# Kernel optimization log

Hardware: AMD Instinct MI355X
Metric: run time of the kernel (lower is better)

The kernel has to match this reference:

```python
import jax, jax.numpy as jnp
import numpy as np

EPS = 1e-5  # BatchNorm1d default eps


def setup_inputs() -> dict:
    key = jax.random.key(0)
    k1, k2 = jax.random.split(key)
    b, d, h, w = 32, 256, 32, 128
    x = jax.random.normal(k1, (b, d, h, w), dtype=jnp.float32)
    # mask=True means padded/masked position (excluded from stats, left untouched)
    mask = jax.random.randint(k2, (b, 1, h, w), 0, 2).astype(bool)
    gamma = jnp.ones((d,), dtype=jnp.float32)
    beta = jnp.zeros((d,), dtype=jnp.float32)
    return {"x": x, "mask": mask, "gamma": gamma, "beta": beta}


def reference(x, mask, gamma, beta):
    # x: [b, d, h, w], mask: [b, 1, h, w] (True = masked)
    not_mask = ~mask[:, 0]                      # [b, h, w]
    wgt = not_mask.astype(x.dtype)              # [b, h, w]
    count = jnp.maximum(wgt.sum(), jnp.asarray(1.0, x.dtype))
    xt = jnp.transpose(x, (0, 2, 3, 1))         # [b, h, w, d]
    wm = wgt[..., None]                         # [b, h, w, 1]
    # masked per-channel batch statistics (biased variance, as BN training mode)
    mean = (xt * wm).sum(axis=(0, 1, 2)) / count                  # [d]
    var = (wm * (xt - mean) ** 2).sum(axis=(0, 1, 2)) / count     # [d]
    normed = (xt - mean) * jax.lax.rsqrt(var + EPS) * gamma + beta
    out = jnp.where(not_mask[..., None], normed, xt)              # scatter-back
    return jnp.transpose(out, (0, 3, 1, 2))     # [b, d, h, w]
```

## Files before the change

kernel.cpp:

```cpp
#include <hip/hip_runtime.h>

#define BB 32
#define DD 256
#define HW 4096
#define DHW (DD * HW)
#define TOTAL (BB * DHW)
#define NSLICE (BB * DD)
#define EPS 1e-5f

typedef float floatx4 __attribute__((ext_vector_type(4)));


__global__ void __launch_bounds__(256)
stats_kernel(const float* __restrict__ x, const int* __restrict__ mask,
             float* __restrict__ ws) {
    const int slice = blockIdx.x;
    const int b = slice >> 8;
    const int d = slice & 255;
    const float4* xs = reinterpret_cast<const float4*>(
        x + (size_t)b * DHW + (size_t)d * HW);
    const int4* ms = reinterpret_cast<const int4*>(mask + b * HW);
    const int tid = threadIdx.x;

    float sum = 0.f, sq = 0.f, cnt = 0.f;
#pragma unroll
    for (int j = 0; j < 4; ++j) {
        const int v = j * 256 + tid;
        float4 xv = xs[v];
        int4 mv = ms[v];
        if (!mv.x) { sum += xv.x; sq += xv.x * xv.x; cnt += 1.f; }
        if (!mv.y) { sum += xv.y; sq += xv.y * xv.y; cnt += 1.f; }
        if (!mv.z) { sum += xv.z; sq += xv.z * xv.z; cnt += 1.f; }
        if (!mv.w) { sum += xv.w; sq += xv.w * xv.w; cnt += 1.f; }
    }

#pragma unroll
    for (int off = 32; off > 0; off >>= 1) {
        sum += __shfl_down(sum, off);
        sq  += __shfl_down(sq, off);
        cnt += __shfl_down(cnt, off);
    }

    __shared__ float ssum[4], ssq[4], scnt[4];
    const int wave = tid >> 6, lane = tid & 63;
    if (lane == 0) { ssum[wave] = sum; ssq[wave] = sq; scnt[wave] = cnt; }
    __syncthreads();
    if (tid == 0) {
        float ts = 0.f, tq = 0.f, tc = 0.f;
#pragma unroll
        for (int i = 0; i < 4; ++i) { ts += ssum[i]; tq += ssq[i]; tc += scnt[i]; }
        ws[slice] = ts;
        ws[NSLICE + slice] = tq;
        if (d == 0) ws[2 * NSLICE + b] = tc;
    }
}

__global__ void __launch_bounds__(256)
apply_kernel(const float* __restrict__ x, const int* __restrict__ mask,
             const float* __restrict__ ws, const float* __restrict__ gamma,
             const float* __restrict__ beta, float* __restrict__ out) {
    __shared__ float s_scale[DD], s_bias[DD];
    const int tid = threadIdx.x;

    float cnt = 0.f;
#pragma unroll
    for (int b = 0; b < BB; ++b) cnt += ws[2 * NSLICE + b];
    cnt = fmaxf(cnt, 1.0f);
    float sum = 0.f, sq = 0.f;
#pragma unroll
    for (int b = 0; b < BB; ++b) {
        sum += ws[b * DD + tid];
        sq  += ws[NSLICE + b * DD + tid];
    }
    const float mean = sum / cnt;
    const float var = fmaxf(sq / cnt - mean * mean, 0.0f);
    const float sc = rsqrtf(var + EPS) * gamma[tid];
    s_scale[tid] = sc;
    s_bias[tid] = beta[tid] - mean * sc;
    __syncthreads();

    const int nvec = TOTAL / 4;
    const int stride = gridDim.x * blockDim.x;
    floatx4* __restrict__ ov = reinterpret_cast<floatx4*>(out);
    for (int v = blockIdx.x * blockDim.x + tid; v < nvec; v += stride) {
        const int e = v << 2;
        const int b = e >> 20;
        const int rem = e & (DHW - 1);
        const int d = rem >> 12;
        const int pos = rem & 4095;
        float4 xv = reinterpret_cast<const float4*>(x)[v];
        int4 mv = reinterpret_cast<const int4*>(mask)[(b * HW + pos) >> 2];
        const float s = s_scale[d], bi = s_bias[d];
        floatx4 o;
        o.x = mv.x ? xv.x : xv.x * s + bi;
        o.y = mv.y ? xv.y : xv.y * s + bi;
        o.z = mv.z ? xv.z : xv.z * s + bi;
        o.w = mv.w ? xv.w : xv.w * s + bi;
        __builtin_nontemporal_store(o, &ov[v]);
    }
}

extern "C" void kernel_launch(void* const* d_in, const int* in_sizes, int n_in,
                              void* d_out, int out_size, void* d_ws, size_t ws_size,
                              hipStream_t stream) {
    const float* x     = (const float*)d_in[0];
    const int*   mask  = (const int*)d_in[1];
    const float* gamma = (const float*)d_in[2];
    const float* beta  = (const float*)d_in[3];
    float* out = (float*)d_out;
    float* ws  = (float*)d_ws;

    stats_kernel<<<NSLICE, 256, 0, stream>>>(x, mask, ws);
    apply_kernel<<<2048, 256, 0, stream>>>(x, mask, ws, gamma, beta, out);
}
```

Before: 70.00 us.

## Fuse stats and apply into one per-channel kernel with block-level reduction

Replaces the two-kernel stats/apply pipeline with a single kernel where each 1024-thread block owns one channel. The block reduces masked sum, sum of squares and count across all batches, computes scale and bias, then re-reads the same channel data to write the normalized output. This removes the workspace round-trip and the second launch, and aims to serve the second read of x from cache instead of HBM. In exchange, the grid is only 256 large blocks with one block per channel, which limits occupancy and latency hiding, and any benefit from the re-read depends on the cache holding the data.

New measurement: 64.93 us (median of 2 runs). 7.2% less time.

```diff
diff --git a/kernel.cpp b/kernel.cpp
--- a/kernel.cpp
+++ b/kernel.cpp
@@ -4,99 +4,74 @@
 #define DD 256
 #define HW 4096
 #define DHW (DD * HW)
-#define TOTAL (BB * DHW)
-#define NSLICE (BB * DD)
 #define EPS 1e-5f
 
 typedef float floatx4 __attribute__((ext_vector_type(4)));
 
+__global__ void __launch_bounds__(1024)
+channel_kernel(const float* __restrict__ x, const int* __restrict__ mask,
+               const float* __restrict__ gamma, const float* __restrict__ beta,
+               float* __restrict__ out) {
+    const int d = blockIdx.x;
+    const int tid = threadIdx.x;
+    const int wave = tid >> 6, lane = tid & 63;
 
-__global__ void __launch_bounds__(256)
-stats_kernel(const float* __restrict__ x, const int* __restrict__ mask,
-             float* __restrict__ ws) {
-    const int slice = blockIdx.x;
-    const int b = slice >> 8;
-    const int d = slice & 255;
-    const float4* xs = reinterpret_cast<const float4*>(
-        x + (size_t)b * DHW + (size_t)d * HW);
-    const int4* ms = reinterpret_cast<const int4*>(mask + b * HW);
-    const int tid = threadIdx.x;
+    const float4* __restrict__ xv4 = reinterpret_cast<const float4*>(x);
+    const int4*   __restrict__ mv4 = reinterpret_cast<const int4*>(mask);
+    const int xbase = d * 1024 + tid;
 
     float sum = 0.f, sq = 0.f, cnt = 0.f;
-#pragma unroll
-    for (int j = 0; j < 4; ++j) {
-        const int v = j * 256 + tid;
-        float4 xv = xs[v];
-        int4 mv = ms[v];
+#pragma unroll 8
+    for (int b = 0; b < BB; ++b) {
+        float4 xv = xv4[b * (DHW / 4) + xbase];
+        int4  mv = mv4[b * 1024 + tid];
         if (!mv.x) { sum += xv.x; sq += xv.x * xv.x; cnt += 1.f; }
         if (!mv.y) { sum += xv.y; sq += xv.y * xv.y; cnt += 1.f; }
         if (!mv.z) { sum += xv.z; sq += xv.z * xv.z; cnt += 1.f; }
         if (!mv.w) { sum += xv.w; sq += xv.w * xv.w; cnt += 1.f; }
     }
 
+    __shared__ float rsum[16], rsq[16], rcnt[16];
+    __shared__ float s_scale, s_bias;
 #pragma unroll
     for (int off = 32; off > 0; off >>= 1) {
         sum += __shfl_down(sum, off);
         sq  += __shfl_down(sq, off);
         cnt += __shfl_down(cnt, off);
     }
+    if (lane == 0) { rsum[wave] = sum; rsq[wave] = sq; rcnt[wave] = cnt; }
+    __syncthreads();
+    if (tid < 16) {
+        float ts = rsum[tid], tq = rsq[tid], tc = rcnt[tid];
+#pragma unroll
+        for (int off = 8; off > 0; off >>= 1) {
+            ts += __shfl_down(ts, off, 16);
+            tq += __shfl_down(tq, off, 16);
+            tc += __shfl_down(tc, off, 16);
+        }
+        if (tid == 0) {
+            tc = fmaxf(tc, 1.0f);
+            const float mean = ts / tc;
+            const float var = fmaxf(tq / tc - mean * mean, 0.0f);
+            const float sc = rsqrtf(var + EPS) * gamma[d];
+            s_scale = sc;
+            s_bias = beta[d] - mean * sc;
+        }
+    }
+    __syncthreads();
+    const float sc = s_scale, bi = s_bias;
 
-    __shared__ float ssum[4], ssq[4], scnt[4];
-    const int wave = tid >> 6, lane = tid & 63;
-    if (lane == 0) { ssum[wave] = sum; ssq[wave] = sq; scnt[wave] = cnt; }
-    __syncthreads();
-    if (tid == 0) {
-        float ts = 0.f, tq = 0.f, tc = 0.f;
-#pragma unroll
-        for (int i = 0; i < 4; ++i) { ts += ssum[i]; tq += ssq[i]; tc += scnt[i]; }
-        ws[slice] = ts;
-        ws[NSLICE + slice] = tq;
-        if (d == 0) ws[2 * NSLICE + b] = tc;
-    }
-}
-
-__global__ void __launch_bounds__(256)
-apply_kernel(const float* __restrict__ x, const int* __restrict__ mask,
-             const float* __restrict__ ws, const float* __restrict__ gamma,
-             const float* __restrict__ beta, float* __restrict__ out) {
-    __shared__ float s_scale[DD], s_bias[DD];
-    const int tid = threadIdx.x;
-
-    float cnt = 0.f;
-#pragma unroll
-    for (int b = 0; b < BB; ++b) cnt += ws[2 * NSLICE + b];
-    cnt = fmaxf(cnt, 1.0f);
-    float sum = 0.f, sq = 0.f;
-#pragma unroll
+    floatx4* __restrict__ ov4 = reinterpret_cast<floatx4*>(out);
+#pragma unroll 8
     for (int b = 0; b < BB; ++b) {
-        sum += ws[b * DD + tid];
-        sq  += ws[NSLICE + b * DD + tid];
-    }
-    const float mean = sum / cnt;
-    const float var = fmaxf(sq / cnt - mean * mean, 0.0f);
-    const float sc = rsqrtf(var + EPS) * gamma[tid];
-    s_scale[tid] = sc;
-    s_bias[tid] = beta[tid] - mean * sc;
-    __syncthreads();
-
-    const int nvec = TOTAL / 4;
-    const int stride = gridDim.x * blockDim.x;
-    floatx4* __restrict__ ov = reinterpret_cast<floatx4*>(out);
-    for (int v = blockIdx.x * blockDim.x + tid; v < nvec; v += stride) {
-        const int e = v << 2;
-        const int b = e >> 20;
-        const int rem = e & (DHW - 1);
-        const int d = rem >> 12;
-        const int pos = rem & 4095;
-        float4 xv = reinterpret_cast<const float4*>(x)[v];
-        int4 mv = reinterpret_cast<const int4*>(mask)[(b * HW + pos) >> 2];
-        const float s = s_scale[d], bi = s_bias[d];
+        float4 xv = xv4[b * (DHW / 4) + xbase];
+        int4  mv = mv4[b * 1024 + tid];
         floatx4 o;
-        o.x = mv.x ? xv.x : xv.x * s + bi;
-        o.y = mv.y ? xv.y : xv.y * s + bi;
-        o.z = mv.z ? xv.z : xv.z * s + bi;
-        o.w = mv.w ? xv.w : xv.w * s + bi;
-        __builtin_nontemporal_store(o, &ov[v]);
+        o.x = mv.x ? xv.x : xv.x * sc + bi;
+        o.y = mv.y ? xv.y : xv.y * sc + bi;
+        o.z = mv.z ? xv.z : xv.z * sc + bi;
+        o.w = mv.w ? xv.w : xv.w * sc + bi;
+        __builtin_nontemporal_store(o, &ov4[b * (DHW / 4) + xbase]);
     }
 }
 
@@ -108,8 +83,6 @@
     const float* gamma = (const float*)d_in[2];
     const float* beta  = (const float*)d_in[3];
     float* out = (float*)d_out;
-    float* ws  = (float*)d_ws;
 
-    stats_kernel<<<NSLICE, 256, 0, stream>>>(x, mask, ws);
-    apply_kernel<<<2048, 256, 0, stream>>>(x, mask, ws, gamma, beta, out);
+    channel_kernel<<<DD, 1024, 0, stream>>>(x, mask, gamma, beta, out);
 }
```
